# Optimization experiments

Hardware: AMD Instinct MI355X
Metric: run time of the kernel (lower is better)

The kernel has to match this reference:

```python
import jax, jax.numpy as jnp
import numpy as np

N_NODES = 100000
N_EDGES = 1600000
IN_F = 128
N_HEADS = 8
HEAD_D = 8  # n_hidden // n_heads = 64 // 8
NEG_SLOPE = 0.2


def setup_inputs() -> dict:
    key = jax.random.key(0)
    k1, k2, k3, k4, k5 = jax.random.split(key, 5)
    vert = jax.random.normal(k1, (N_NODES, IN_F), dtype=jnp.float32)
    edge = jax.random.randint(k2, (2, N_EDGES), 0, N_NODES, dtype=jnp.int64)
    scale_w = 1.0 / np.sqrt(IN_F)
    W = jax.random.normal(k3, (IN_F, N_HEADS, HEAD_D), dtype=jnp.float32) * scale_w
    scale_a = 1.0 / np.sqrt(HEAD_D)
    a_src = jax.random.normal(k4, (N_HEADS, HEAD_D), dtype=jnp.float32) * scale_a
    a_dst = jax.random.normal(k5, (N_HEADS, HEAD_D), dtype=jnp.float32) * scale_a
    return {"vert": vert, "edge": edge, "W": W, "a_src": a_src, "a_dst": a_dst}


def reference(vert, edge, W, a_src, a_dst):
    # Per-head linear projection: [N, H, D]
    g = jnp.einsum('nf,fhd->nhd', vert, W)
    src, dst = edge[0], edge[1]
    # Decomposed attention logits: e_ij = LeakyReLU(a_src.g_i + a_dst.g_j)
    e_s = jnp.sum(g * a_src[None], axis=-1)  # [N, H]
    e_d = jnp.sum(g * a_dst[None], axis=-1)  # [N, H]
    scores = jax.nn.leaky_relu(e_s[src] + e_d[dst], NEG_SLOPE)  # [E, H]
    # Segment softmax over incoming edges of each destination node
    m = jax.ops.segment_max(scores, dst, num_segments=N_NODES)  # [N, H]
    m = jnp.where(jnp.isneginf(m), 0.0, m)
    ex = jnp.exp(scores - m[dst])  # [E, H]
    denom = jax.ops.segment_sum(ex, dst, num_segments=N_NODES)  # [N, H]
    alpha = ex / jnp.maximum(denom[dst], 1e-16)  # [E, H]
    # Weighted message aggregation: scatter-add alpha * g[src] into dst
    msg = alpha[:, :, None] * g[src]  # [E, H, D]
    agg = jax.ops.segment_sum(msg, dst, num_segments=N_NODES)  # [N, H, D]
    out = agg.reshape(N_NODES, N_HEADS * HEAD_D)  # concat heads
    # GAT_DE trailing ELU (dropout=0.0 -> identity)
    return jax.nn.elu(out)
```

## Files before the change

kernel.cpp:

```cpp
#include <hip/hip_runtime.h>
#include <hip/hip_bf16.h>
#include <hip/hip_fp16.h>
#include <math.h>

#define N_NODES 100000
#define N_EDGES 1600000
#define IN_F    128
#define NH      8
#define HD      8
#define HID     64
#define NEG_SLOPE 0.2f

#define BSH   5
#define BSZ   32
#define NBK   3125
#define BCAPG 704
#define BCAP  832
#define NBPJ  782
#define NPB   160
#define EPB   10000

typedef short bf16x8 __attribute__((ext_vector_type(8)));
typedef float f32x4  __attribute__((ext_vector_type(4)));

static __device__ __forceinline__ unsigned short f2bf(float x) {
    __hip_bfloat16 h = __float2bfloat16(x);
    return *(unsigned short*)&h;
}

__global__ __launch_bounds__(256) void prep_kernel(
    const float* __restrict__ W, const float* __restrict__ a_src,
    const float* __restrict__ a_dst, unsigned short* __restrict__ Bg,
    int* __restrict__ gcnt)
{
    const int tid = threadIdx.x;
    for (int i = blockIdx.x * 256 + tid; i < NBK; i += 16 * 256) gcnt[i] = 0;
    if (blockIdx.x != 0) return;

    __shared__ __align__(16) unsigned short bl[10240];
    for (int idx = tid; idx < 128 * 16; idx += 256) {
        const int f = idx >> 4, cq = idx & 15;
        const float4 w = *(const float4*)(W + f * 64 + cq * 4);
        const int kc = f >> 5, q = (f >> 3) & 3, j = f & 7;
        const float wf[4] = {w.x, w.y, w.z, w.w};
        #pragma unroll
        for (int i = 0; i < 4; ++i) {
            const int col = cq * 4 + i;
            bl[(col >> 4) * 2048 + kc * 512 + q * 128 + (col & 15) * 8 + j] = f2bf(wf[i]);
        }
    }
    for (int idx = tid; idx < 128 * 8; idx += 256) {
        const int f = idx >> 3, h = idx & 7;
        const float4 wa = *(const float4*)(W + f * 64 + h * 8);
        const float4 wb = *(const float4*)(W + f * 64 + h * 8 + 4);
        const float4 sa = *(const float4*)(a_src + h * 8);
        const float4 sb = *(const float4*)(a_src + h * 8 + 4);
        const float4 da = *(const float4*)(a_dst + h * 8);
        const float4 db = *(const float4*)(a_dst + h * 8 + 4);
        float esv = fmaf(wa.x, sa.x, fmaf(wa.y, sa.y, fmaf(wa.z, sa.z,
                    fmaf(wa.w, sa.w, fmaf(wb.x, sb.x, fmaf(wb.y, sb.y,
                    fmaf(wb.z, sb.z, wb.w * sb.w)))))));
        float edv = fmaf(wa.x, da.x, fmaf(wa.y, da.y, fmaf(wa.z, da.z,
                    fmaf(wa.w, da.w, fmaf(wb.x, db.x, fmaf(wb.y, db.y,
                    fmaf(wb.z, db.z, wb.w * db.w)))))));
        const int kc = f >> 5, q = (f >> 3) & 3, j = f & 7;
        bl[4 * 2048 + kc * 512 + q * 128 + h * 8 + j]       = f2bf(esv);
        bl[4 * 2048 + kc * 512 + q * 128 + (8 + h) * 8 + j] = f2bf(edv);
    }
    __syncthreads();
    for (int idx = tid; idx < 1280; idx += 256)
        ((uint4*)Bg)[idx] = ((const uint4*)bl)[idx];
}

__global__ __launch_bounds__(512) void fused_pp_kernel(
    const float* __restrict__ vert, const unsigned short* __restrict__ Bg,
    __hip_bfloat16* __restrict__ gb, float* __restrict__ es, float* __restrict__ ed,
    const int* __restrict__ edge, int* __restrict__ gcnt,
    unsigned int* __restrict__ packed)
{
    __shared__ __align__(16) char smem[28672];
    const int tid = threadIdx.x;

    if (blockIdx.x < NBPJ) {
        unsigned short* b_lds = (unsigned short*)smem;
        const int nbeg = blockIdx.x * 128;
        const int lane = tid & 63, wv = tid >> 6;
        const int mn   = lane & 15, quad = lane >> 4;

        for (int idx = tid; idx < 1280; idx += 512)
            *(uint4*)(smem + idx * 16) = ((const uint4*)Bg)[idx];

        const int row = nbeg + wv * 16 + mn;
        bf16x8 afr[4];
        #pragma unroll
        for (int kc = 0; kc < 4; ++kc) {
            float4 p = make_float4(0.f, 0.f, 0.f, 0.f);
            float4 q4 = make_float4(0.f, 0.f, 0.f, 0.f);
            if (row < N_NODES) {
                const float* rp = vert + (size_t)row * IN_F + kc * 32 + quad * 8;
                p  = *(const float4*)rp;
                q4 = *(const float4*)(rp + 4);
            }
            bf16x8 a;
            a[0] = (short)f2bf(p.x);  a[1] = (short)f2bf(p.y);
            a[2] = (short)f2bf(p.z);  a[3] = (short)f2bf(p.w);
            a[4] = (short)f2bf(q4.x); a[5] = (short)f2bf(q4.y);
            a[6] = (short)f2bf(q4.z); a[7] = (short)f2bf(q4.w);
            afr[kc] = a;
        }
        __syncthreads();

        const unsigned short* bbase = b_lds + quad * 128 + mn * 8;
        f32x4 acc[5];
        #pragma unroll
        for (int c = 0; c < 5; ++c) acc[c] = (f32x4){0.f, 0.f, 0.f, 0.f};
        #pragma unroll
        for (int kc = 0; kc < 4; ++kc) {
            #pragma unroll
            for (int c = 0; c < 5; ++c) {
                const bf16x8 bfr = *(const bf16x8*)(bbase + c * 2048 + kc * 512);
                acc[c] = __builtin_amdgcn_mfma_f32_16x16x32_bf16(afr[kc], bfr, acc[c], 0, 0, 0);
            }
        }
        __syncthreads();

        unsigned short* gl = (unsigned short*)smem + wv * 1152;
        float* lesd = (float*)(smem + 18432) + wv * 320;
        #pragma unroll
        for (int c = 0; c < 4; ++c)
            #pragma unroll
            for (int r = 0; r < 4; ++r)
                gl[(quad * 4 + r) * 72 + c * 16 + mn] = f2bf(acc[c][r]);
        {
            float* dst = (mn < 8) ? (lesd + mn) : (lesd + 160 + (mn - 8));
            #pragma unroll
            for (int r = 0; r < 4; ++r) dst[(quad * 4 + r) * 10] = acc[4][r];
        }
        __syncthreads();
        {
            const int row2 = lane >> 2, part = lane & 3;
            const int node = nbeg + wv * 16 + row2;
            if (node < N_NODES) {
                const uint4* sp = (const uint4*)(gl + row2 * 72 + part * 16);
                *(uint4*)((unsigned short*)gb + (size_t)node * HID + part * 16) = sp[0];
                *(uint4*)((unsigned short*)gb + (size_t)node * HID + part * 16 + 8) = sp[1];
            }
        }
        {
            const int nl = lane >> 2, h2 = (lane & 3) * 2;
            const int node = nbeg + wv * 16 + nl;
            if (node < N_NODES) {
                *(float2*)(es + node * NH + h2) = *(const float2*)(lesd + nl * 10 + h2);
                *(float2*)(ed + node * NH + h2) = *(const float2*)(lesd + 160 + nl * 10 + h2);
            }
        }
    } else {
        int* lh    = (int*)smem;
        int* lbase = (int*)(smem + 12544);
        const int pb = blockIdx.x - NBPJ;

        for (int i = tid; i < NBK; i += 512) lh[i] = 0;
        __syncthreads();
        const int4* src4 = (const int4*)(edge + pb * EPB);
        const int4* dst4 = (const int4*)(edge + N_EDGES + pb * EPB);
        for (int t = tid; t < EPB / 4; t += 512) {
            const int4 d = dst4[t];
            atomicAdd(&lh[d.x >> BSH], 1);
            atomicAdd(&lh[d.y >> BSH], 1);
            atomicAdd(&lh[d.z >> BSH], 1);
            atomicAdd(&lh[d.w >> BSH], 1);
        }
        __syncthreads();
        for (int i = tid; i < NBK; i += 512) {
            const int c = lh[i];
            lbase[i] = c ? (i * BCAPG + atomicAdd(&gcnt[i], c)) : 0;
            lh[i] = 0;
        }
        __syncthreads();
        for (int t = tid; t < EPB / 4; t += 512) {
            const int4 s = src4[t];
            const int4 d = dst4[t];
            int bk, pos;
            bk = d.x >> BSH; pos = min(lbase[bk] + atomicAdd(&lh[bk], 1), NBK * BCAPG - 1);
            packed[pos] = ((unsigned)s.x << BSH) | (d.x & (BSZ - 1));
            bk = d.y >> BSH; pos = min(lbase[bk] + atomicAdd(&lh[bk], 1), NBK * BCAPG - 1);
            packed[pos] = ((unsigned)s.y << BSH) | (d.y & (BSZ - 1));
            bk = d.z >> BSH; pos = min(lbase[bk] + atomicAdd(&lh[bk], 1), NBK * BCAPG - 1);
            packed[pos] = ((unsigned)s.z << BSH) | (d.z & (BSZ - 1));
            bk = d.w >> BSH; pos = min(lbase[bk] + atomicAdd(&lh[bk], 1), NBK * BCAPG - 1);
            packed[pos] = ((unsigned)s.w << BSH) | (d.w & (BSZ - 1));
        }
    }
}

__global__ __launch_bounds__(256) void p2agg_kernel(
    const int* __restrict__ gcnt, const unsigned int* __restrict__ packed,
    const unsigned short* __restrict__ gb, const float* __restrict__ es,
    const float* __restrict__ ed, float* __restrict__ out)
{
    __shared__ unsigned int ssrt[BCAP];
    __shared__ __align__(16) unsigned short pexp[BCAP * 8];
    __shared__ int ldeg[BSZ], loffs[BSZ];
    __shared__ __align__(16) float led[BSZ * NH];
    unsigned int* epk = (unsigned int*)pexp;

    const int tid  = threadIdx.x;
    const int b    = blockIdx.x;
    const int nbeg = b << BSH;
    const int ebase = b * BCAPG;
    const int ecnt  = min(gcnt[b], BCAP);

    if (tid < BSZ) ldeg[tid] = 0;
    for (int i = tid; i < BSZ * NH; i += 256) led[i] = ed[nbeg * NH + i];
    __syncthreads();

    for (int i = tid; i < ecnt; i += 256) {
        const unsigned int p = packed[ebase + i];
        epk[i] = p;
        atomicAdd(&ldeg[p & (BSZ - 1)], 1);
    }
    __syncthreads();

    if (tid < BSZ) {
        int v = ldeg[tid];
        #pragma unroll
        for (int off = 1; off < BSZ; off <<= 1) {
            const int t = __shfl_up(v, off, 64);
            if (tid >= off) v += t;
        }
        loffs[tid] = v - ldeg[tid];
    }
    __syncthreads();

    for (int i = tid; i < ecnt; i += 256) {
        const unsigned int p = epk[i];
        const int pos = atomicAdd(&loffs[p & (BSZ - 1)], 1);
        ssrt[pos] = ((p >> BSH) << 7) | (p & (BSZ - 1));
    }
    __syncthreads();

    for (int i = tid; i < ecnt; i += 256) {
        const unsigned pw = ssrt[i];
        const int src = (int)(pw >> 7), dl = (int)(pw & (BSZ - 1));
        const float4 e0 = *(const float4*)(es + (size_t)src * NH);
        const float4 e1 = *(const float4*)(es + (size_t)src * NH + 4);
        const float4 l0 = *(const float4*)(led + dl * NH);
        const float4 l1 = *(const float4*)(led + dl * NH + 4);
        float s[8] = {e0.x + l0.x, e0.y + l0.y, e0.z + l0.z, e0.w + l0.w,
                      e1.x + l1.x, e1.y + l1.y, e1.z + l1.z, e1.w + l1.w};
        #pragma unroll
        for (int k = 0; k < 8; ++k)
            s[k] = __expf(fmaxf(s[k], s[k] * NEG_SLOPE));
        __half2 h01 = __floats2half2_rn(s[0], s[1]);
        __half2 h23 = __floats2half2_rn(s[2], s[3]);
        __half2 h45 = __floats2half2_rn(s[4], s[5]);
        __half2 h67 = __floats2half2_rn(s[6], s[7]);
        uint4 w;
        w.x = *(unsigned*)&h01; w.y = *(unsigned*)&h23;
        w.z = *(unsigned*)&h45; w.w = *(unsigned*)&h67;
        *(uint4*)(pexp + i * 8) = w;
    }
    __syncthreads();

    const int lane  = tid & 63;
    const int wv    = tid >> 6;
    const int c2    = lane & 31;
    const int khalf = lane >> 5;
    const int h     = c2 >> 2;
    const unsigned c2_4 = (unsigned)(c2 << 2);
    const char* gbase = (const char*)gb;

#define BULK_STEP(s, pw)                                                      \
    {                                                                         \
        const float pe = __half2float(                                        \
            *(const __half*)(pexp + ((i + 2 * (s) + khalf) << 3) + h));       \
        const unsigned voff = ((pw) & ~127u) | c2_4;                          \
        const unsigned gu = *(const unsigned*)(gbase + voff);                 \
        acc0 = fmaf(pe, __uint_as_float(gu << 16), acc0);                     \
        acc1 = fmaf(pe, __uint_as_float(gu & 0xFFFF0000u), acc1);             \
        l += pe;                                                              \
    }

    for (int n = wv; n < BSZ; n += 4) {
        const int end = loffs[n];
        const int beg = end - ldeg[n];
        float l = 0.f, acc0 = 0.f, acc1 = 0.f;
        int i = beg;
        for (; i + 8 <= end; i += 8) {
            const unsigned pw0 = ssrt[i + khalf];
            const unsigned pw1 = ssrt[i + 2 + khalf];
            const unsigned pw2 = ssrt[i + 4 + khalf];
            const unsigned pw3 = ssrt[i + 6 + khalf];
            BULK_STEP(0, pw0); BULK_STEP(1, pw1);
            BULK_STEP(2, pw2); BULK_STEP(3, pw3);
        }
        if (i < end) {
            #pragma unroll
            for (int s = 0; s < 4; ++s) {
                const int e  = i + 2 * s + khalf;
                const int ec = min(e, end - 1);
                const unsigned pw = ssrt[ec];
                float pe = __half2float(*(const __half*)(pexp + (ec << 3) + h));
                pe = (e < end) ? pe : 0.f;
                const unsigned voff = (pw & ~127u) | c2_4;
                const unsigned gu = *(const unsigned*)(gbase + voff);
                acc0 = fmaf(pe, __uint_as_float(gu << 16), acc0);
                acc1 = fmaf(pe, __uint_as_float(gu & 0xFFFF0000u), acc1);
                l += pe;
            }
        }
        l    += __shfl_xor(l, 32);
        acc0 += __shfl_xor(acc0, 32);
        acc1 += __shfl_xor(acc1, 32);
        const float rl = 1.f / fmaxf(l, 1e-16f);
        float o0 = acc0 * rl, o1 = acc1 * rl;
        o0 = (o0 > 0.f) ? o0 : (__expf(o0) - 1.f);
        o1 = (o1 > 0.f) ? o1 : (__expf(o1) - 1.f);
        const float ov = khalf ? o1 : o0;
        out[(size_t)(nbeg + n) * HID + c2 * 2 + khalf] = ov;
    }
#undef BULK_STEP
}

extern "C" void kernel_launch(void* const* d_in, const int* in_sizes, int n_in,
                              void* d_out, int out_size, void* d_ws, size_t ws_size,
                              hipStream_t stream)
{
    const float* vert  = (const float*)d_in[0];
    const int*   edge  = (const int*)  d_in[1];
    const float* W     = (const float*)d_in[2];
    const float* a_src = (const float*)d_in[3];
    const float* a_dst = (const float*)d_in[4];
    float* out = (float*)d_out;

    char* ws = (char*)d_ws;
    __hip_bfloat16* gb     = (__hip_bfloat16*)(ws);
    float*          es     = (float*)(ws + 12800000);
    float*          ed     = (float*)(ws + 16000000);
    unsigned int*   packed = (unsigned int*)(ws + 19200000);
    int*            gcnt   = (int*)(ws + 28000000);
    unsigned short* Bg     = (unsigned short*)(ws + 28012544);

    prep_kernel<<<16, 256, 0, stream>>>(W, a_src, a_dst, Bg, gcnt);
    fused_pp_kernel<<<NBPJ + NPB, 512, 0, stream>>>(
        vert, Bg, gb, es, ed, edge, gcnt, packed);
    p2agg_kernel<<<NBK, 256, 0, stream>>>(gcnt, packed, (const unsigned short*)gb, es, ed, out);
}
```

Baseline: 180.9 us.

## Replace single-pass fine bucketing with two-level coarse bucket plus radix refine kernel

```diff
diff --git a/kernel.cpp b/kernel.cpp
--- a/kernel.cpp
+++ b/kernel.cpp
@@ -14,11 +14,13 @@
 #define BSH   5
 #define BSZ   32
 #define NBK   3125
-#define BCAPG 704
+#define NCB   196
+#define CSTR  9216
 #define BCAP  832
 #define NBPJ  782
 #define NPB   160
 #define EPB   10000
+#define GSTR  16
 
 typedef short bf16x8 __attribute__((ext_vector_type(8)));
 typedef float f32x4  __attribute__((ext_vector_type(4)));
@@ -34,7 +36,7 @@
     int* __restrict__ gcnt)
 {
     const int tid = threadIdx.x;
-    for (int i = blockIdx.x * 256 + tid; i < NBK; i += 16 * 256) gcnt[i] = 0;
+    for (int i = blockIdx.x * 256 + tid; i < NCB * GSTR; i += 16 * 256) gcnt[i] = 0;
     if (blockIdx.x != 0) return;
 
     __shared__ __align__(16) unsigned short bl[10240];
@@ -156,45 +158,87 @@
         }
     } else {
         int* lh    = (int*)smem;
-        int* lbase = (int*)(smem + 12544);
+        int* lbase = (int*)(smem + 1024);
         const int pb = blockIdx.x - NBPJ;
 
-        for (int i = tid; i < NBK; i += 512) lh[i] = 0;
+        if (tid < NCB) lh[tid] = 0;
         __syncthreads();
         const int4* src4 = (const int4*)(edge + pb * EPB);
         const int4* dst4 = (const int4*)(edge + N_EDGES + pb * EPB);
         for (int t = tid; t < EPB / 4; t += 512) {
             const int4 d = dst4[t];
-            atomicAdd(&lh[d.x >> BSH], 1);
-            atomicAdd(&lh[d.y >> BSH], 1);
-            atomicAdd(&lh[d.z >> BSH], 1);
-            atomicAdd(&lh[d.w >> BSH], 1);
-        }
-        __syncthreads();
-        for (int i = tid; i < NBK; i += 512) {
-            const int c = lh[i];
-            lbase[i] = c ? (i * BCAPG + atomicAdd(&gcnt[i], c)) : 0;
-            lh[i] = 0;
+            atomicAdd(&lh[d.x >> 9], 1);
+            atomicAdd(&lh[d.y >> 9], 1);
+            atomicAdd(&lh[d.z >> 9], 1);
+            atomicAdd(&lh[d.w >> 9], 1);
+        }
+        __syncthreads();
+        if (tid < NCB) {
+            const int c = lh[tid];
+            lbase[tid] = c ? (tid * CSTR + atomicAdd(&gcnt[tid * GSTR], c)) : 0;
+            lh[tid] = 0;
         }
         __syncthreads();
         for (int t = tid; t < EPB / 4; t += 512) {
             const int4 s = src4[t];
             const int4 d = dst4[t];
             int bk, pos;
-            bk = d.x >> BSH; pos = min(lbase[bk] + atomicAdd(&lh[bk], 1), NBK * BCAPG - 1);
-            packed[pos] = ((unsigned)s.x << BSH) | (d.x & (BSZ - 1));
-            bk = d.y >> BSH; pos = min(lbase[bk] + atomicAdd(&lh[bk], 1), NBK * BCAPG - 1);
-            packed[pos] = ((unsigned)s.y << BSH) | (d.y & (BSZ - 1));
-            bk = d.z >> BSH; pos = min(lbase[bk] + atomicAdd(&lh[bk], 1), NBK * BCAPG - 1);
-            packed[pos] = ((unsigned)s.z << BSH) | (d.z & (BSZ - 1));
-            bk = d.w >> BSH; pos = min(lbase[bk] + atomicAdd(&lh[bk], 1), NBK * BCAPG - 1);
-            packed[pos] = ((unsigned)s.w << BSH) | (d.w & (BSZ - 1));
-        }
+            bk = d.x >> 9; pos = min(lbase[bk] + atomicAdd(&lh[bk], 1), NCB * CSTR - 1);
+            packed[pos] = ((unsigned)s.x << 9) | (unsigned)(d.x & 511);
+            bk = d.y >> 9; pos = min(lbase[bk] + atomicAdd(&lh[bk], 1), NCB * CSTR - 1);
+            packed[pos] = ((unsigned)s.y << 9) | (unsigned)(d.y & 511);
+            bk = d.z >> 9; pos = min(lbase[bk] + atomicAdd(&lh[bk], 1), NCB * CSTR - 1);
+            packed[pos] = ((unsigned)s.z << 9) | (unsigned)(d.z & 511);
+            bk = d.w >> 9; pos = min(lbase[bk] + atomicAdd(&lh[bk], 1), NCB * CSTR - 1);
+            packed[pos] = ((unsigned)s.w << 9) | (unsigned)(d.w & 511);
+        }
+    }
+}
+
+__global__ __launch_bounds__(512) void radixb_kernel(
+    const int* __restrict__ gcnt, unsigned int* __restrict__ packed,
+    int2* __restrict__ finfo)
+{
+    __shared__ unsigned int ebuf[CSTR];
+    __shared__ unsigned int stage[CSTR];
+    __shared__ int fh[16], fpre[16];
+    const int tid = threadIdx.x;
+    const int cb  = blockIdx.x;
+    const int cnt = min(gcnt[cb * GSTR], CSTR);
+    unsigned int* in = packed + (size_t)cb * CSTR;
+
+    if (tid < 16) fh[tid] = 0;
+    __syncthreads();
+    for (int i = tid; i < cnt; i += 512) {
+        const unsigned v = in[i];
+        ebuf[i] = v;
+        atomicAdd(&fh[(v >> 5) & 15], 1);
+    }
+    __syncthreads();
+    if (tid == 0) {
+        int s = 0;
+        #pragma unroll
+        for (int f = 0; f < 16; ++f) { fpre[f] = s; s += fh[f]; }
+    }
+    __syncthreads();
+    if (tid < 16) fh[tid] = fpre[tid];
+    __syncthreads();
+    for (int i = tid; i < cnt; i += 512) {
+        const unsigned v = ebuf[i];
+        const int pos = atomicAdd(&fh[(v >> 5) & 15], 1);
+        stage[pos] = ((v >> 9) << 7) | (v & 31);
+    }
+    __syncthreads();
+    for (int i = tid; i < cnt; i += 512) in[i] = stage[i];
+    if (tid < 16) {
+        const int fg = cb * 16 + tid;
+        if (fg < NBK)
+            finfo[fg] = make_int2(cb * CSTR + fpre[tid], fh[tid] - fpre[tid]);
     }
 }
 
 __global__ __launch_bounds__(256) void p2agg_kernel(
-    const int* __restrict__ gcnt, const unsigned int* __restrict__ packed,
+    const int2* __restrict__ finfo, const unsigned int* __restrict__ packed,
     const unsigned short* __restrict__ gb, const float* __restrict__ es,
     const float* __restrict__ ed, float* __restrict__ out)
 {
@@ -207,8 +251,9 @@
     const int tid  = threadIdx.x;
     const int b    = blockIdx.x;
     const int nbeg = b << BSH;
-    const int ebase = b * BCAPG;
-    const int ecnt  = min(gcnt[b], BCAP);
+    const int2 fi  = finfo[b];
+    const int ebase = fi.x;
+    const int ecnt  = min(fi.y, BCAP);
 
     if (tid < BSZ) ldeg[tid] = 0;
     for (int i = tid; i < BSZ * NH; i += 256) led[i] = ed[nbeg * NH + i];
@@ -235,7 +280,7 @@
     for (int i = tid; i < ecnt; i += 256) {
         const unsigned int p = epk[i];
         const int pos = atomicAdd(&loffs[p & (BSZ - 1)], 1);
-        ssrt[pos] = ((p >> BSH) << 7) | (p & (BSZ - 1));
+        ssrt[pos] = p;
     }
     __syncthreads();
 
@@ -338,11 +383,13 @@
     float*          es     = (float*)(ws + 12800000);
     float*          ed     = (float*)(ws + 16000000);
     unsigned int*   packed = (unsigned int*)(ws + 19200000);
-    int*            gcnt   = (int*)(ws + 28000000);
-    unsigned short* Bg     = (unsigned short*)(ws + 28012544);
+    int*            gcnt   = (int*)(ws + 26425344);
+    int2*           finfo  = (int2*)(ws + 26437888);
+    unsigned short* Bg     = (unsigned short*)(ws + 26462896);
 
     prep_kernel<<<16, 256, 0, stream>>>(W, a_src, a_dst, Bg, gcnt);
     fused_pp_kernel<<<NBPJ + NPB, 512, 0, stream>>>(
         vert, Bg, gb, es, ed, edge, gcnt, packed);
-    p2agg_kernel<<<NBK, 256, 0, stream>>>(gcnt, packed, (const unsigned short*)gb, es, ed, out);
-}
+    radixb_kernel<<<NCB, 512, 0, stream>>>(gcnt, packed, finfo);
+    p2agg_kernel<<<NBK, 256, 0, stream>>>(finfo, packed, (const unsigned short*)gb, es, ed, out);
+}
```

New measurement: 177.2 us. 2.1% less time.
